# Kernel tuning notes

Measured on AMD Instinct MI355X. Metric: run time of the kernel, lower is better.

Reference implementation:

```python
import jax, jax.numpy as jnp
import numpy as np

B, L, D, H, DH, S_POKES = 1, 4096, 1024, 16, 64, 3072


def setup_inputs() -> dict:
    key = jax.random.key(0)
    k0, k1, k2, k3 = jax.random.split(key, 4)
    x = jax.random.normal(k0, (B, L, D), jnp.float32)
    pos = jax.random.uniform(k1, (B, L, 2), jnp.float32)  # positions in [0,1]^2
    qkv_w = jax.random.normal(k2, (3 * D, D), jnp.float32) * 0.02
    out_w = jax.random.normal(k3, (D, D), jnp.float32) * 0.02
    scale = jnp.ones((H,), jnp.float32) * 10.0  # per-head cosine-sim scale (init 10)
    # AxialRoPE2D freq table: logspace(pi, 10*pi), view(2, d_head//4, n_heads).mT
    n = H * DH // 4
    f = np.exp(np.linspace(np.log(np.pi), np.log(10.0 * np.pi), n + 1)[:-1])
    freqs = jnp.asarray(np.stack([f, f]).reshape(2, DH // 4, H).transpose(0, 2, 1), jnp.float32)
    return {"x": x, "pos": pos, "qkv_w": qkv_w, "out_w": out_w,
            "scale": scale, "freqs": freqs, "n_pokes": S_POKES}


def _cos_scale(q, k, scale, eps=1e-8):
    # scale_for_cosine_sim: qk logits = scale * cosine_similarity
    sq = jnp.sum(q * q, axis=-1, keepdims=True)
    sk = jnp.sum(k * k, axis=-1, keepdims=True)
    ss = jnp.sqrt(jnp.abs(scale) + eps)
    return q * (ss * jax.lax.rsqrt(sq + eps)), k * (ss * jax.lax.rsqrt(sk + eps))


def _axial_theta(pos, freqs):
    # pos [B,L,2] in [0,1]; theta [B,H,L,DH//2]
    th_w = (pos[..., None, 0:1] * 2.0 - 1.0) * freqs[0]  # [B,L,H,DH//4]
    th_h = (pos[..., None, 1:2] * 2.0 - 1.0) * freqs[1]
    return jnp.concatenate([th_h, th_w], axis=-1).transpose(0, 2, 1, 3)


def _rope(x, theta):
    d = theta.shape[-1]  # DH//2 -> rotates the full head dim, x3 part empty
    x1, x2 = x[..., :d], x[..., d:2 * d]
    cos, sin = jnp.cos(theta), jnp.sin(theta)
    return jnp.concatenate([x1 * cos - x2 * sin, x2 * cos + x1 * sin], axis=-1)


def reference(x, pos, qkv_w, out_w, scale, freqs, n_pokes):
    b, l, dm = x.shape
    qkv = x @ qkv_w.T                          # [B,L,3D]
    q, k, v = jnp.split(qkv, 3, axis=-1)
    split_heads = lambda t: t.reshape(b, l, H, DH).transpose(0, 2, 1, 3)  # [B,H,L,DH]
    q, k, v = split_heads(q), split_heads(k), split_heads(v)
    q, k = _cos_scale(q, k, scale.reshape(1, H, 1, 1))
    theta = _axial_theta(pos, freqs)
    q, k = _rope(q, theta), _rope(k, theta)
    s = n_pokes
    qp, kp, vp = q[:, :, :s], k[:, :, :s], v[:, :, :s]
    qq, kq, vq = q[:, :, s:], k[:, :, s:], v[:, :, s:]
    # pokes: causal self-attention (scale=1.0, cosine-sim logits)
    sc_pp = jnp.einsum('bhqd,bhkd->bhqk', qp, kp)
    causal = jnp.tril(jnp.ones((s, s), bool))
    p_pp = jax.nn.softmax(jnp.where(causal, sc_pp, -jnp.inf), axis=-1)
    out_p = jnp.einsum('bhqk,bhkd->bhqd', p_pp, vp)
    # queries: attend to all pokes + themselves (diagonal), never each other
    sc_qp = jnp.einsum('bhqd,bhkd->bhqk', qq, kp)          # [B,H,Q,S]
    sc_self = jnp.sum(qq * kq, axis=-1, keepdims=True)     # [B,H,Q,1]
    p_q = jax.nn.softmax(jnp.concatenate([sc_qp, sc_self], axis=-1), axis=-1)
    out_q = jnp.einsum('bhqk,bhkd->bhqd', p_q[..., :s], vp) + p_q[..., s:] * vq
    out = jnp.concatenate([out_p, out_q], axis=2).transpose(0, 2, 1, 3).reshape(b, l, dm)
    return out @ out_w.T
```

## Files before the change

### kernel.cpp

```cpp
#include <hip/hip_runtime.h>
#include <math.h>

#define SEQL   4096
#define DMODEL 1024
#define NH     16
#define DHEAD  64
#define SPOKES 3072
#define NQUERY (SEQL - SPOKES)
#define QKVN   (3 * DMODEL)

typedef short bf16x8 __attribute__((ext_vector_type(8)));
typedef short bf16x4 __attribute__((ext_vector_type(4)));
typedef float f32x4  __attribute__((ext_vector_type(4)));

__device__ __forceinline__ short f2bf(float f) {
    unsigned u = __builtin_bit_cast(unsigned, f);
    u += 0x7fffu + ((u >> 16) & 1u);
    return (short)(u >> 16);
}
__device__ __forceinline__ float bf2f(short s) {
    unsigned u = ((unsigned)(unsigned short)s) << 16;
    return __builtin_bit_cast(float, u);
}
__device__ __forceinline__ unsigned cvt_pk_bf16(float lo, float hi) {
    unsigned u;
    asm("v_cvt_pk_bf16_f32 %0, %1, %2" : "=v"(u) : "v"(lo), "v"(hi));
    return u;
}
__device__ __forceinline__ int swz(int row) { return ((row & 7) ^ (row >> 3)) << 4; }

__device__ __forceinline__ void gload_lds16(const void* g, void* l) {
    __builtin_amdgcn_global_load_lds(
        (const __attribute__((address_space(1))) unsigned int*)g,
        (__attribute__((address_space(3))) unsigned int*)l,
        16, 0, 0);
}

__global__ __launch_bounds__(256) void cvt_f32_bf16(
    const float* __restrict__ in, short* __restrict__ out, int n8)
{
    const int i = blockIdx.x * 256 + threadIdx.x;
    if (i >= n8) return;
    float4 a = ((const float4*)in)[i * 2];
    float4 b = ((const float4*)in)[i * 2 + 1];
    bf16x8 v;
    v[0] = f2bf(a.x); v[1] = f2bf(a.y); v[2] = f2bf(a.z); v[3] = f2bf(a.w);
    v[4] = f2bf(b.x); v[5] = f2bf(b.y); v[6] = f2bf(b.z); v[7] = f2bf(b.w);
    ((bf16x8*)out)[i] = v;
}

template<bool BF16OUT>
__global__ __launch_bounds__(256) void gemm_bf16(
    const short* __restrict__ A, const short* __restrict__ B, void* __restrict__ Cv,
    int K, int ldc)
{
    __shared__ short As[128 * 64];
    __shared__ short Bs[128 * 64];

    const int t = threadIdx.x;
    const int lane = t & 63, w = t >> 6;
    const int c = lane & 15, g = lane >> 4;
    const int wr = w >> 1, wc = w & 1;
    const int m0 = blockIdx.y * 128, n0 = blockIdx.x * 128;

    f32x4 acc[4][4] = {};

    for (int k0 = 0; k0 < K; k0 += 64) {
        __syncthreads();
        #pragma unroll
        for (int i = 0; i < 4; ++i) {
            const int chunk = (w * 4 + i) * 64 + lane;
            const int row = chunk >> 3, cc = chunk & 7;
            gload_lds16(A + (size_t)(m0 + row) * K + k0 + cc * 8,
                        As + (size_t)(w * 4 + i) * 512);
            gload_lds16(B + (size_t)(n0 + row) * K + k0 + cc * 8,
                        Bs + (size_t)(w * 4 + i) * 512);
        }
        __syncthreads();

        #pragma unroll
        for (int kk = 0; kk < 2; ++kk) {
            bf16x8 af[4], bf[4];
            #pragma unroll
            for (int i = 0; i < 4; ++i)
                af[i] = *(const bf16x8*)(As + (wr * 64 + i * 16 + c) * 64 + kk * 32 + g * 8);
            #pragma unroll
            for (int j = 0; j < 4; ++j)
                bf[j] = *(const bf16x8*)(Bs + (wc * 64 + j * 16 + c) * 64 + kk * 32 + g * 8);
            #pragma unroll
            for (int i = 0; i < 4; ++i)
                #pragma unroll
                for (int j = 0; j < 4; ++j)
                    acc[i][j] = __builtin_amdgcn_mfma_f32_16x16x32_bf16(af[i], bf[j], acc[i][j], 0, 0, 0);
        }
    }

    #pragma unroll
    for (int i = 0; i < 4; ++i)
        #pragma unroll
        for (int r = 0; r < 4; ++r) {
            const int row = m0 + wr * 64 + i * 16 + g * 4 + r;
            #pragma unroll
            for (int j = 0; j < 4; ++j) {
                const int col = n0 + wc * 64 + j * 16 + c;
                const float v = acc[i][j][r];
                if (BF16OUT) ((short*)Cv)[(size_t)row * ldc + col] = f2bf(v);
                else         ((float*)Cv)[(size_t)row * ldc + col] = v;
            }
        }
}

__global__ __launch_bounds__(256) void transform_qk(
    short* __restrict__ qkv, const float* __restrict__ pos,
    const float* __restrict__ scale, const float* __restrict__ freqs)
{
    const int w    = threadIdx.x >> 6;
    const int lane = threadIdx.x & 63;
    const int rid  = blockIdx.x * 4 + w;
    const int l    = rid >> 4;
    const int h    = rid & 15;

    short* qp = qkv + (size_t)l * QKVN + h * DHEAD;
    short* kp = qp + DMODEL;

    float q = bf2f(qp[lane]);
    float k = bf2f(kp[lane]);

    float sq = q * q, sk = k * k;
    #pragma unroll
    for (int o = 32; o > 0; o >>= 1) {
        sq += __shfl_xor(sq, o);
        sk += __shfl_xor(sk, o);
    }
    const float ss = sqrtf(fabsf(scale[h]) + 1e-8f);
    q *= ss * rsqrtf(sq + 1e-8f);
    k *= ss * rsqrtf(sk + 1e-8f);

    const int   j  = lane & 31;
    const float p  = pos[l * 2 + (j < 16 ? 1 : 0)];
    const float fj = (j < 16) ? freqs[256 + h * 16 + j] : freqs[h * 16 + (j - 16)];
    const float th = (p * 2.0f - 1.0f) * fj;
    const float cs = cosf(th), sn = sinf(th);

    const float qo = __shfl_xor(q, 32);
    const float ko = __shfl_xor(k, 32);
    const float qr = (lane < 32) ? q * cs - qo * sn : q * cs + qo * sn;
    const float kr = (lane < 32) ? k * cs - ko * sn : k * cs + ko * sn;

    qp[lane] = f2bf(qr);
    kp[lane] = f2bf(kr);
}

__global__ __launch_bounds__(256) void attn_fused(
    const short* __restrict__ qkv, short* __restrict__ attn,
    short* __restrict__ pacc_c, float* __restrict__ pml_c, float* __restrict__ pml0_c,
    short* __restrict__ pacc_q, float* __restrict__ pml_q, float* __restrict__ pml0_q)
{
    __shared__ short Kl[2][64 * 64];
    __shared__ short VTl[2][64 * 64];
    __shared__ short Pl[4][16 * 64];

    const int h = blockIdx.y;
    const int t = threadIdx.x, lane = t & 63, w = t >> 6;
    const int c = lane & 15, g = lane >> 4;
    const int qcol = h * DHEAD, kcol = DMODEL + h * DHEAD, vcol = 2 * DMODEL + h * DHEAD;

    const int xc = blockIdx.x;
    bool causal; int z, NS, q0, kt0, ktn, qt = 0, qb = 0;
    if (xc < 48) {
        causal = false; qb = xc / 3; z = xc - qb * 3; NS = 3;
        q0 = SPOKES + qb * 64; kt0 = z * 16; ktn = 16;
    } else {
        causal = true;
        if (xc < 96)       { const int i = xc - 48; qt = 47 - i / 3; z = i - (i / 3) * 3; NS = 3; }
        else if (xc < 128) { const int i = xc - 96; qt = 31 - (i >> 1); z = i & 1; NS = 2; }
        else               { qt = 143 - xc; z = 0; NS = 1; }
        q0 = qt * 64;
        const int full = qt + 1, b = full / NS, r = full - b * NS;
        kt0 = z * b + (z < r ? z : r);
        ktn = b + (z < r ? 1 : 0);
    }

    const int qg = q0 + w * 16 + c;

    bf16x8 qf0, qf1;
    {
        const short* qrow = qkv + (size_t)qg * QKVN + qcol;
        qf0 = *(const bf16x8*)(qrow + g * 8);
        qf1 = *(const bf16x8*)(qrow + 32 + g * 8);
    }

    float m = -INFINITY, l = 0.0f;
    f32x4 acc[4] = {};
    bf16x8 vregA, vregB;

    auto KDMA = [&](int buf, int kt) {
        const int k0 = kt * 64;
        #pragma unroll
        for (int i = 0; i < 2; ++i) {
            const int ch = i * 256 + t;
            const int kv = ch >> 3, s = ch & 7;
            const int o = s ^ ((kv & 7) ^ (kv >> 3));
            gload_lds16(qkv + (size_t)(k0 + kv) * QKVN + kcol + o * 8,
                        (char*)Kl[buf] + i * 4096 + w * 1024);
        }
    };
    auto VLOAD = [&](int kt) {
        const int k0 = kt * 64;
        const short* v0 = qkv + (size_t)(k0 + 2 * (t >> 3)) * QKVN + vcol + (t & 7) * 8;
        vregA = *(const bf16x8*)v0;
        vregB = *(const bf16x8*)(v0 + QKVN);
    };
    auto VWRITE = [&](int buf) {
        const int p2 = t >> 3, oc = t & 7;
        #pragma unroll
        for (int j = 0; j < 8; ++j) {
            const int d = oc * 8 + j;
            const unsigned u = ((unsigned)(unsigned short)vregA[j]) |
                               (((unsigned)(unsigned short)vregB[j]) << 16);
            *(unsigned*)((char*)VTl[buf] + d * 128 + ((4 * p2) ^ swz(d))) = u;
        }
    };

    VLOAD(kt0);
    KDMA(0, kt0);
    VWRITE(0);
    __syncthreads();

    for (int it = 0; it < ktn; ++it) {
        const int kt = kt0 + it;
        const int cur = it & 1, nxt = cur ^ 1;
        const int k0 = kt * 64;

        if (it + 1 < ktn) { VLOAD(kt + 1); KDMA(nxt, kt + 1); }

        f32x4 st[4];
        #pragma unroll
        for (int mt = 0; mt < 4; ++mt) {
            const int kvr = mt * 16 + c;
            bf16x8 ka = *(const bf16x8*)((const char*)Kl[cur] + kvr * 128 + ((g * 16) ^ swz(kvr)));
            bf16x8 kb = *(const bf16x8*)((const char*)Kl[cur] + kvr * 128 + ((64 + g * 16) ^ swz(kvr)));
            f32x4 zz = {0.f, 0.f, 0.f, 0.f};
            zz = __builtin_amdgcn_mfma_f32_16x16x32_bf16(ka, qf0, zz, 0, 0, 0);
            st[mt] = __builtin_amdgcn_mfma_f32_16x16x32_bf16(kb, qf1, zz, 0, 0, 0);
        }

        if (causal && (k0 + 63 > q0 + w * 16)) {
            #pragma unroll
            for (int mt = 0; mt < 4; ++mt)
                #pragma unroll
                for (int r = 0; r < 4; ++r)
                    if (k0 + mt * 16 + g * 4 + r > qg) st[mt][r] = -INFINITY;
        }
        float tmax = -INFINITY;
        #pragma unroll
        for (int mt = 0; mt < 4; ++mt)
            #pragma unroll
            for (int r = 0; r < 4; ++r) tmax = fmaxf(tmax, st[mt][r]);
        tmax = fmaxf(tmax, __shfl_xor(tmax, 16));
        tmax = fmaxf(tmax, __shfl_xor(tmax, 32));
        if (__any(tmax > m + 8.0f)) {
            const float mnew = fmaxf(m, tmax);
            const float pfac = __expf(m - mnew);
            l *= pfac;
            #pragma unroll
            for (int dt = 0; dt < 4; ++dt)
                #pragma unroll
                for (int r = 0; r < 4; ++r) acc[dt][r] *= pfac;
            m = mnew;
        }
        {
            const float mref = m;
            float rs = 0.0f;
            #pragma unroll
            for (int mt = 0; mt < 4; ++mt) {
                const float e0 = __expf(st[mt][0] - mref);
                const float e1 = __expf(st[mt][1] - mref);
                const float e2 = __expf(st[mt][2] - mref);
                const float e3 = __expf(st[mt][3] - mref);
                rs += (e0 + e1) + (e2 + e3);
                uint2 u;
                u.x = cvt_pk_bf16(e0, e1);
                u.y = cvt_pk_bf16(e2, e3);
                *(uint2*)((char*)Pl[w] + c * 128 + ((mt * 32 + g * 8) ^ swz(c))) = u;
            }
            rs += __shfl_xor(rs, 16);
            rs += __shfl_xor(rs, 32);
            l += rs;
        }

        #pragma unroll
        for (int kc = 0; kc < 2; ++kc) {
            bf16x8 pb = *(const bf16x8*)((const char*)Pl[w] + c * 128 + ((kc * 64 + g * 16) ^ swz(c)));
            #pragma unroll
            for (int dt = 0; dt < 4; ++dt) {
                const int d = dt * 16 + c;
                bf16x8 vf = *(const bf16x8*)((const char*)VTl[cur] + d * 128 + ((kc * 64 + g * 16) ^ swz(d)));
                acc[dt] = __builtin_amdgcn_mfma_f32_16x16x32_bf16(vf, pb, acc[dt], 0, 0, 0);
            }
        }

        if (it + 1 < ktn) VWRITE(nxt);
        __syncthreads();
    }

    if (!causal && z == 0) {
        float ss = 0.0f;
        {
            const short* krow = qkv + (size_t)qg * QKVN + kcol;
            bf16x8 k0s = *(const bf16x8*)(krow + g * 8);
            bf16x8 k1s = *(const bf16x8*)(krow + 32 + g * 8);
            #pragma unroll
            for (int j = 0; j < 8; ++j)
                ss += bf2f(qf0[j]) * bf2f(k0s[j]) + bf2f(qf1[j]) * bf2f(k1s[j]);
            ss += __shfl_xor(ss, 16);
            ss += __shfl_xor(ss, 32);
        }
        const float mnew = fmaxf(m, ss);
        const float pf = __expf(m - mnew);
        const float ps = __expf(ss - mnew);
        const short* vrow = qkv + (size_t)qg * QKVN + vcol;
        #pragma unroll
        for (int dt = 0; dt < 4; ++dt) {
            bf16x4 vs = *(const bf16x4*)(vrow + dt * 16 + g * 4);
            #pragma unroll
            for (int r = 0; r < 4; ++r)
                acc[dt][r] = acc[dt][r] * pf + ps * bf2f(vs[r]);
        }
        l = l * pf + ps;
        m = mnew;
    }

    if (causal && NS == 1) {
        const float inv = 1.0f / l;
        short* orow = attn + (size_t)qg * DMODEL + qcol;
        #pragma unroll
        for (int dt = 0; dt < 4; ++dt)
            #pragma unroll
            for (int r = 0; r < 4; ++r)
                orow[dt * 16 + g * 4 + r] = f2bf(acc[dt][r] * inv);
    } else if (z == 0) {
        float* pml0 = causal ? pml0_c : pml0_q;
        const int stride = causal ? 2048 : 1024;
        const int base   = causal ? 1024 : SPOKES;
        short* orow = attn + (size_t)qg * DMODEL + qcol;
        #pragma unroll
        for (int dt = 0; dt < 4; ++dt)
            #pragma unroll
            for (int r = 0; r < 4; ++r)
                orow[dt * 16 + g * 4 + r] = f2bf(acc[dt][r]);
        if (g == 0) {
            float* p = pml0 + ((size_t)h * stride + (qg - base)) * 2;
            p[0] = m;
            p[1] = l;
        }
    } else {
        const int slot = causal ? (qt < 32 ? qt - 16 : 16 + (qt - 32) * 2 + (z - 1))
                                : qb * 2 + (z - 1);
        short* pacc = causal ? pacc_c : pacc_q;
        float* pml  = causal ? pml_c  : pml_q;
        const int rl = w * 16 + c;
        short* prow = pacc + ((size_t)slot * 64 + rl) * DMODEL + qcol;
        #pragma unroll
        for (int dt = 0; dt < 4; ++dt)
            #pragma unroll
            for (int r = 0; r < 4; ++r)
                prow[dt * 16 + g * 4 + r] = f2bf(acc[dt][r]);
        if (g == 0) {
            float* p = pml + ((size_t)(slot * 16 + h) * 64 + rl) * 2;
            p[0] = m;
            p[1] = l;
        }
    }
}

__global__ __launch_bounds__(256) void attn_combine(
    short* __restrict__ attn, const float* __restrict__ pml0,
    const short* __restrict__ pacc, const float* __restrict__ pml,
    int rowbase, int pml0_stride, int pml0_off,
    int slotBase, int slotMul, int nextra)
{
    const int i = blockIdx.x * 256 + threadIdx.x;
    const int r = i >> 7;
    const int h = (i >> 3) & 15;
    const int o = i & 7;

    const float* p0 = pml0 + ((size_t)h * pml0_stride + pml0_off + r) * 2;
    const float m0 = p0[0], l0 = p0[1];
    float M = m0;
    float me[2], le[2];
    for (int e = 0; e < nextra; ++e) {
        const int slot = slotBase + (r >> 6) * slotMul + e;
        const float* p = pml + ((size_t)(slot * 16 + h) * 64 + (r & 63)) * 2;
        me[e] = p[0]; le[e] = p[1];
        M = fmaxf(M, me[e]);
    }
    const float w0 = __expf(m0 - M);
    float L = w0 * l0;
    float we[2];
    for (int e = 0; e < nextra; ++e) { we[e] = __expf(me[e] - M); L += we[e] * le[e]; }

    short* arow = attn + (size_t)(rowbase + r) * DMODEL + h * 64 + o * 8;
    bf16x8 a0 = *(const bf16x8*)arow;
    float outv[8];
    #pragma unroll
    for (int j = 0; j < 8; ++j) outv[j] = w0 * bf2f(a0[j]);
    for (int e = 0; e < nextra; ++e) {
        const int slot = slotBase + (r >> 6) * slotMul + e;
        bf16x8 a = *(const bf16x8*)(pacc + ((size_t)slot * 64 + (r & 63)) * DMODEL + h * 64 + o * 8);
        #pragma unroll
        for (int j = 0; j < 8; ++j) outv[j] += we[e] * bf2f(a[j]);
    }
    const float inv = 1.0f / L;
    bf16x8 res;
    #pragma unroll
    for (int j = 0; j < 8; ++j) res[j] = f2bf(outv[j] * inv);
    *(bf16x8*)arow = res;
}

extern "C" void kernel_launch(void* const* d_in, const int* in_sizes, int n_in,
                              void* d_out, int out_size, void* d_ws, size_t ws_size,
                              hipStream_t stream)
{
    const float* x      = (const float*)d_in[0];
    const float* pos    = (const float*)d_in[1];
    const float* qkv_w  = (const float*)d_in[2];
    const float* out_w  = (const float*)d_in[3];
    const float* scale  = (const float*)d_in[4];
    const float* freqs  = (const float*)d_in[5];
    float*       out    = (float*)d_out;

    const size_t MB = 1024 * 1024;
    char* ws = (char*)d_ws;
    short* qkv_bf  = (short*)(ws);
    short* x_bf    = (short*)(ws + 24 * MB);
    short* wqkv_bf = (short*)(ws + 32 * MB);
    short* wout_bf = (short*)(ws + 38 * MB);
    short* pacc_c  = (short*)(ws + 40 * MB);
    float* pml_c   = (float*)(ws + 46 * MB);
    float* pml0_c  = (float*)(ws + 46 * MB + 393216);
    short* attn_bf = x_bf;
    short* pacc_q  = wqkv_bf;
    float* pml_q   = (float*)((char*)wqkv_bf + 4194304);
    float* pml0_q  = (float*)((char*)wqkv_bf + 4456448);

    const dim3 blk(256);

    cvt_f32_bf16<<<dim3(SEQL * DMODEL / 8 / 256), blk, 0, stream>>>(x, x_bf, SEQL * DMODEL / 8);
    cvt_f32_bf16<<<dim3(QKVN * DMODEL / 8 / 256), blk, 0, stream>>>(qkv_w, wqkv_bf, QKVN * DMODEL / 8);
    cvt_f32_bf16<<<dim3(DMODEL * DMODEL / 8 / 256), blk, 0, stream>>>(out_w, wout_bf, DMODEL * DMODEL / 8);

    gemm_bf16<true><<<dim3(QKVN / 128, SEQL / 128), blk, 0, stream>>>(
        x_bf, wqkv_bf, qkv_bf, DMODEL, QKVN);

    transform_qk<<<dim3(SEQL * NH / 4), blk, 0, stream>>>(qkv_bf, pos, scale, freqs);

    attn_fused<<<dim3(144, NH), blk, 0, stream>>>(
        qkv_bf, attn_bf, pacc_c, pml_c, pml0_c, pacc_q, pml_q, pml0_q);

    attn_combine<<<dim3(512), blk, 0, stream>>>(attn_bf, pml0_c, pacc_c, pml_c,
                                                1024, 2048, 0,    0, 1, 1);
    attn_combine<<<dim3(512), blk, 0, stream>>>(attn_bf, pml0_c, pacc_c, pml_c,
                                                2048, 2048, 1024, 16, 2, 2);
    attn_combine<<<dim3(512), blk, 0, stream>>>(attn_bf, pml0_q, pacc_q, pml_q,
                                                SPOKES, 1024, 0,  0, 2, 2);

    gemm_bf16<false><<<dim3(DMODEL / 128, SEQL / 128), blk, 0, stream>>>(
        attn_bf, wout_bf, out, DMODEL, DMODEL);
}
```

Baseline: 203.4 us.

## Single-buffer K/V tiles in LDS to raise occupancy and add MFMA priority

Replaces the double-buffered K and V^T LDS tiles with single buffers, adding barriers so the next K tile is DMA'd after QK^T and V^T is rewritten after PV. Launch bounds now request 6 blocks per SM and the MFMA sections are wrapped in s_setprio raises. The aim is to cut LDS and register footprint so more waves are resident and hide latency. In exchange it adds an extra barrier per iteration and removes the overlap of the next tile's loads with the current compute.

After: 309.3 us. +52.0%, slower.

```diff
diff --git a/kernel.cpp b/kernel.cpp
--- a/kernel.cpp
+++ b/kernel.cpp
@@ -151,13 +151,13 @@
     kp[lane] = f2bf(kr);
 }
 
-__global__ __launch_bounds__(256) void attn_fused(
+__global__ __launch_bounds__(256, 6) void attn_fused(
     const short* __restrict__ qkv, short* __restrict__ attn,
     short* __restrict__ pacc_c, float* __restrict__ pml_c, float* __restrict__ pml0_c,
     short* __restrict__ pacc_q, float* __restrict__ pml_q, float* __restrict__ pml0_q)
 {
-    __shared__ short Kl[2][64 * 64];
-    __shared__ short VTl[2][64 * 64];
+    __shared__ short Kl[64 * 64];
+    __shared__ short VTl[64 * 64];
     __shared__ short Pl[4][16 * 64];
 
     const int h = blockIdx.y;
@@ -194,7 +194,7 @@
     f32x4 acc[4] = {};
     bf16x8 vregA, vregB;
 
-    auto KDMA = [&](int buf, int kt) {
+    auto KDMA = [&](int kt) {
         const int k0 = kt * 64;
         #pragma unroll
         for (int i = 0; i < 2; ++i) {
@@ -202,7 +202,7 @@
             const int kv = ch >> 3, s = ch & 7;
             const int o = s ^ ((kv & 7) ^ (kv >> 3));
             gload_lds16(qkv + (size_t)(k0 + kv) * QKVN + kcol + o * 8,
-                        (char*)Kl[buf] + i * 4096 + w * 1024);
+                        (char*)Kl + i * 4096 + w * 1024);
         }
     };
     auto VLOAD = [&](int kt) {
@@ -211,39 +211,41 @@
         vregA = *(const bf16x8*)v0;
         vregB = *(const bf16x8*)(v0 + QKVN);
     };
-    auto VWRITE = [&](int buf) {
+    auto VWRITE = [&]() {
         const int p2 = t >> 3, oc = t & 7;
         #pragma unroll
         for (int j = 0; j < 8; ++j) {
             const int d = oc * 8 + j;
             const unsigned u = ((unsigned)(unsigned short)vregA[j]) |
                                (((unsigned)(unsigned short)vregB[j]) << 16);
-            *(unsigned*)((char*)VTl[buf] + d * 128 + ((4 * p2) ^ swz(d))) = u;
+            *(unsigned*)((char*)VTl + d * 128 + ((4 * p2) ^ swz(d))) = u;
         }
     };
 
     VLOAD(kt0);
-    KDMA(0, kt0);
-    VWRITE(0);
+    KDMA(kt0);
+    VWRITE();
     __syncthreads();
 
     for (int it = 0; it < ktn; ++it) {
         const int kt = kt0 + it;
-        const int cur = it & 1, nxt = cur ^ 1;
         const int k0 = kt * 64;
 
-        if (it + 1 < ktn) { VLOAD(kt + 1); KDMA(nxt, kt + 1); }
-
         f32x4 st[4];
+        __builtin_amdgcn_s_setprio(1);
         #pragma unroll
         for (int mt = 0; mt < 4; ++mt) {
             const int kvr = mt * 16 + c;
-            bf16x8 ka = *(const bf16x8*)((const char*)Kl[cur] + kvr * 128 + ((g * 16) ^ swz(kvr)));
-            bf16x8 kb = *(const bf16x8*)((const char*)Kl[cur] + kvr * 128 + ((64 + g * 16) ^ swz(kvr)));
+            bf16x8 ka = *(const bf16x8*)((const char*)Kl + kvr * 128 + ((g * 16) ^ swz(kvr)));
+            bf16x8 kb = *(const bf16x8*)((const char*)Kl + kvr * 128 + ((64 + g * 16) ^ swz(kvr)));
             f32x4 zz = {0.f, 0.f, 0.f, 0.f};
             zz = __builtin_amdgcn_mfma_f32_16x16x32_bf16(ka, qf0, zz, 0, 0, 0);
             st[mt] = __builtin_amdgcn_mfma_f32_16x16x32_bf16(kb, qf1, zz, 0, 0, 0);
         }
+        __builtin_amdgcn_s_setprio(0);
+
+        __syncthreads();
+        if (it + 1 < ktn) { KDMA(kt + 1); VLOAD(kt + 1); }
 
         if (causal && (k0 + 63 > q0 + w * 16)) {
             #pragma unroll
@@ -289,19 +291,24 @@
             l += rs;
         }
 
+        __builtin_amdgcn_s_setprio(1);
         #pragma unroll
         for (int kc = 0; kc < 2; ++kc) {
             bf16x8 pb = *(const bf16x8*)((const char*)Pl[w] + c * 128 + ((kc * 64 + g * 16) ^ swz(c)));
             #pragma unroll
             for (int dt = 0; dt < 4; ++dt) {
                 const int d = dt * 16 + c;
-                bf16x8 vf = *(const bf16x8*)((const char*)VTl[cur] + d * 128 + ((kc * 64 + g * 16) ^ swz(d)));
+                bf16x8 vf = *(const bf16x8*)((const char*)VTl + d * 128 + ((kc * 64 + g * 16) ^ swz(d)));
                 acc[dt] = __builtin_amdgcn_mfma_f32_16x16x32_bf16(vf, pb, acc[dt], 0, 0, 0);
             }
         }
-
-        if (it + 1 < ktn) VWRITE(nxt);
+        __builtin_amdgcn_s_setprio(0);
+
         __syncthreads();
+        if (it + 1 < ktn) {
+            VWRITE();
+            __syncthreads();
+        }
     }
 
     if (!causal && z == 0) {
```
